# Optimization experiments

Measured on AMD Instinct MI355X. Metric: run time of the kernel, lower is better.

## Reference

```python
import jax, jax.numpy as jnp
import numpy as np

IN_F = 256
OUT_F = 256
HYPER = 128
BATCH = 4096


def setup_inputs() -> dict:
    key = jax.random.key(0)
    ks = jax.random.split(key, 9)
    s_in = 1.0 / np.sqrt(IN_F)
    s_h = 1.0 / np.sqrt(HYPER)
    x = jax.random.normal(ks[0], (BATCH, IN_F), dtype=jnp.float32)
    # weight_gen: Linear(in, hyper) -> ReLU -> Linear(hyper, in*out)
    W1g = jax.random.uniform(ks[1], (IN_F, HYPER), jnp.float32, -s_in, s_in)
    b1g = jax.random.uniform(ks[2], (HYPER,), jnp.float32, -s_in, s_in)
    W2g = jax.random.uniform(ks[3], (HYPER, IN_F * OUT_F), jnp.float32, -s_h, s_h)
    b2g = jax.random.uniform(ks[4], (IN_F * OUT_F,), jnp.float32, -s_h, s_h)
    # bias_gen: Linear(in, hyper) -> ReLU -> Linear(hyper, out)
    W1b = jax.random.uniform(ks[5], (IN_F, HYPER), jnp.float32, -s_in, s_in)
    b1b = jax.random.uniform(ks[6], (HYPER,), jnp.float32, -s_in, s_in)
    W2b = jax.random.uniform(ks[7], (HYPER, OUT_F), jnp.float32, -s_h, s_h)
    b2b = jax.random.uniform(ks[8], (OUT_F,), jnp.float32, -s_h, s_h)
    return {"x": x, "W1g": W1g, "b1g": b1g, "W2g": W2g, "b2g": b2g,
            "W1b": W1b, "b1b": b1b, "W2b": W2b, "b2b": b2b}


def reference(x, W1g, b1g, W2g, b2g, W1b, b1b, W2b, b2b):
    B = x.shape[0]
    # generate per-sample weights [B, out, in]
    hg = jax.nn.relu(x @ W1g + b1g)                      # [B, hyper]
    weights = (hg @ W2g + b2g).reshape(B, OUT_F, IN_F)   # [B, out, in]
    # generate per-sample bias [B, out]
    hb = jax.nn.relu(x @ W1b + b1b)                      # [B, hyper]
    bias = hb @ W2b + b2b                                # [B, out]
    # batched matvec: bmm(weights, x[...,None]) + bias
    out = jnp.einsum('boi,bi->bo', weights, x) + bias    # [B, out]
    return out
```

## Files before the change

kernel.cpp:

```cpp
#include <hip/hip_runtime.h>

#define AS1 __attribute__((address_space(1)))
#define AS3 __attribute__((address_space(3)))

typedef short short8 __attribute__((ext_vector_type(8)));
typedef float f32x16 __attribute__((ext_vector_type(16)));
typedef unsigned short ushort4v __attribute__((ext_vector_type(4)));

#define BATCH 4096
#define IN_F 256
#define OUT_F 256
#define HYP 128
#define HX 129
#define KP (HX * IN_F)

__device__ __forceinline__ float bf2f(unsigned short u) {
  unsigned v = ((unsigned)u) << 16;
  float f;
  __builtin_memcpy(&f, &v, 4);
  return f;
}
__device__ __forceinline__ unsigned short f2bf(float f) {
  unsigned u;
  __builtin_memcpy(&u, &f, 4);
  unsigned r = u + 0x7fffu + ((u >> 16) & 1u);
  return (unsigned short)(r >> 16);
}

__device__ __forceinline__ void gld_lds16(const unsigned short* g, unsigned short* s) {
  __builtin_amdgcn_global_load_lds((const AS1 unsigned int*)g, (AS3 unsigned int*)s, 16, 0, 0);
}

__global__ void k_buildV(const float* __restrict__ W2g, const float* __restrict__ b2g,
                         unsigned short* __restrict__ Vb) {
  const int cid = blockIdx.x * 256 + threadIdx.x;
  const int ic = cid & 31;
  const int pair = cid >> 5;
  const int h = pair % HX;
  const int o = pair / HX;
  const float* src = (h < HYP) ? (W2g + (size_t)h * (OUT_F * IN_F) + o * IN_F + ic * 8)
                               : (b2g + o * IN_F + ic * 8);
  const float4 v0 = ((const float4*)src)[0];
  const float4 v1 = ((const float4*)src)[1];
  uint4 pk;
  pk.x = (unsigned)f2bf(v0.x) | ((unsigned)f2bf(v0.y) << 16);
  pk.y = (unsigned)f2bf(v0.z) | ((unsigned)f2bf(v0.w) << 16);
  pk.z = (unsigned)f2bf(v1.x) | ((unsigned)f2bf(v1.y) << 16);
  pk.w = (unsigned)f2bf(v1.z) | ((unsigned)f2bf(v1.w) << 16);
  *(uint4*)(Vb + (size_t)o * KP + h * IN_F + ic * 8) = pk;
}

__global__ __launch_bounds__(256) void k_pre(const float* __restrict__ x,
                                             const float* __restrict__ W1g, const float* __restrict__ b1g,
                                             const float* __restrict__ W1b, const float* __restrict__ b1b,
                                             const float* __restrict__ W2b, const float* __restrict__ b2b,
                                             unsigned short* __restrict__ hgbT,
                                             unsigned short* __restrict__ xb,
                                             float* __restrict__ out) {
  __shared__ float xl[16 * IN_F];
  __shared__ float hbl[16 * HYP];
  __shared__ unsigned short hgt[HYP * 16];
  const int t = threadIdx.x;
  const int r0 = blockIdx.x * 16;
  for (int j0 = 0; j0 < 16 * IN_F; j0 += 256) {
    const float v = x[(size_t)r0 * IN_F + j0 + t];
    xl[j0 + t] = v;
    xb[(size_t)r0 * IN_F + j0 + t] = f2bf(v);
  }
  __syncthreads();
  const int h = t & 127;
  const int rb = (t >> 7) * 8;
  float ag[8] = {0.f, 0.f, 0.f, 0.f, 0.f, 0.f, 0.f, 0.f};
  float av[8] = {0.f, 0.f, 0.f, 0.f, 0.f, 0.f, 0.f, 0.f};
  for (int i = 0; i < IN_F; ++i) {
    const float wg = W1g[i * HYP + h];
    const float wb = W1b[i * HYP + h];
#pragma unroll
    for (int r = 0; r < 8; ++r) {
      const float xv = xl[(rb + r) * IN_F + i];
      ag[r] += xv * wg;
      av[r] += xv * wb;
    }
  }
  const float bg = b1g[h], bb = b1b[h];
#pragma unroll
  for (int r = 0; r < 8; ++r) {
    float g = ag[r] + bg; g = g > 0.f ? g : 0.f;
    float v = av[r] + bb; v = v > 0.f ? v : 0.f;
    hgt[h * 16 + rb + r] = f2bf(g);
    hbl[(rb + r) * HYP + h] = v;
  }
  __syncthreads();
  {
    const int h2 = t >> 1, part = t & 1;
    const uint4 pk = *(const uint4*)&hgt[h2 * 16 + part * 8];
    *(uint4*)&hgbT[(size_t)h2 * BATCH + r0 + part * 8] = pk;
  }
  float acc[16];
#pragma unroll
  for (int r = 0; r < 16; ++r) acc[r] = 0.f;
  for (int hh = 0; hh < HYP; ++hh) {
    const float w = W2b[hh * OUT_F + t];
#pragma unroll
    for (int r = 0; r < 16; ++r) acc[r] += hbl[r * HYP + hh] * w;
  }
  const float bo = b2b[t];
#pragma unroll
  for (int r = 0; r < 16; ++r) out[(size_t)(r0 + r) * OUT_F + t] = acc[r] + bo;
}

__global__ __launch_bounds__(256, 1) void k_gemm(const unsigned short* __restrict__ Vb,
                                                 const unsigned short* __restrict__ hgbT,
                                                 const unsigned short* __restrict__ xb,
                                                 float* __restrict__ out) {
  __shared__ __align__(16) unsigned short Bl[2][64 * 256];
  __shared__ __align__(16) unsigned short hgs[33 * 256];
  const int tid = threadIdx.x;
  const int lane = tid & 63;
  const int wave = tid >> 6;
  const int l31 = lane & 31;
  const int hi = lane >> 5;
  const int m0 = blockIdx.x * 256;
  const int o0 = blockIdx.y * 64;
  const int z = blockIdx.z;
  const int hBeg = (z * HX) >> 2;
  const int hEnd = ((z + 1) * HX) >> 2;
  const int nh = hEnd - hBeg;

  for (int idx = tid; idx < nh * 256; idx += 256) {
    const int hl = idx >> 8;
    const int hh = hBeg + hl;
    hgs[idx] = (hh == HYP) ? (unsigned short)0x3F80
                           : hgbT[(size_t)hh * BATCH + m0 + (idx & 255)];
  }

  const int mrow0 = m0 + wave * 64 + l31;
  const int mrow1 = mrow0 + 32;
  uint4 xf0[16], xf1[16];
#pragma unroll
  for (int j = 0; j < 16; ++j) {
    xf0[j] = *(const uint4*)(xb + (size_t)mrow0 * IN_F + j * 16 + hi * 8);
    xf1[j] = *(const uint4*)(xb + (size_t)mrow1 * IN_F + j * 16 + hi * 8);
  }

  const int nB = tid >> 5;
  const int p = tid & 31;
  const int cs = p ^ (nB & 7);
  const unsigned short* gsrc = Vb + (size_t)(o0 + nB) * KP + cs * 8 + (size_t)hBeg * IN_F;

  f32x16 zv;
#pragma unroll
  for (int i = 0; i < 16; ++i) zv[i] = 0.0f;
  f32x16 acc00 = zv, acc01 = zv, acc10 = zv, acc11 = zv;
  f32x16 ah00 = zv, ah01 = zv, ah10 = zv, ah11 = zv;

#pragma unroll
  for (int j = 0; j < 8; ++j)
    gld_lds16(gsrc + (size_t)j * 8 * KP, &Bl[0][(tid + 256 * j) * 8]);
  __syncthreads();

  for (int r = 0; r < nh; ++r) {
    const int buf = r & 1;
    if (r + 1 < nh) {
      const unsigned short* gs = gsrc + (size_t)(r + 1) * IN_F;
#pragma unroll
      for (int j = 0; j < 8; ++j)
        gld_lds16(gs + (size_t)j * 8 * KP, &Bl[buf ^ 1][(tid + 256 * j) * 8]);
    }
    float hgf0[16], hgf1[16];
#pragma unroll
    for (int q = 0; q < 4; ++q) {
      const ushort4v v0 = *(const ushort4v*)&hgs[r * 256 + wave * 64 + 4 * hi + q * 8];
      const ushort4v v1 = *(const ushort4v*)&hgs[r * 256 + wave * 64 + 32 + 4 * hi + q * 8];
#pragma unroll
      for (int e = 0; e < 4; ++e) {
        hgf0[q * 4 + e] = bf2f(v0[e]);
        hgf1[q * 4 + e] = bf2f(v1[e]);
      }
    }
    const unsigned short* bp = &Bl[buf][0];
#pragma unroll
    for (int ic = 0; ic < 4; ++ic) {
#pragma unroll
      for (int t = 0; t < 4; ++t) {
        const int c0 = ic * 8 + t * 2 + hi;
        const int pr = c0 ^ (l31 & 7);
        const short8 b0 = *(const short8*)(bp + l31 * 256 + pr * 8);
        const short8 b1 = *(const short8*)(bp + (32 + l31) * 256 + pr * 8);
        const short8 a0 = __builtin_bit_cast(short8, xf0[ic * 4 + t]);
        const short8 a1 = __builtin_bit_cast(short8, xf1[ic * 4 + t]);
        ah00 = __builtin_amdgcn_mfma_f32_32x32x16_bf16(a0, b0, ah00, 0, 0, 0);
        ah01 = __builtin_amdgcn_mfma_f32_32x32x16_bf16(a0, b1, ah01, 0, 0, 0);
        ah10 = __builtin_amdgcn_mfma_f32_32x32x16_bf16(a1, b0, ah10, 0, 0, 0);
        ah11 = __builtin_amdgcn_mfma_f32_32x32x16_bf16(a1, b1, ah11, 0, 0, 0);
      }
    }
#pragma unroll
    for (int g = 0; g < 16; ++g) {
      acc00[g] += hgf0[g] * ah00[g];
      acc01[g] += hgf0[g] * ah01[g];
      acc10[g] += hgf1[g] * ah10[g];
      acc11[g] += hgf1[g] * ah11[g];
    }
    ah00 = zv; ah01 = zv; ah10 = zv; ah11 = zv;
    __syncthreads();
  }

  const int mb = m0 + wave * 64 + 4 * hi;
#pragma unroll
  for (int g = 0; g < 16; ++g) {
    const int row0 = mb + (g & 3) + 8 * (g >> 2);
    atomicAdd(&out[(size_t)row0 * OUT_F + o0 + l31], acc00[g]);
    atomicAdd(&out[(size_t)row0 * OUT_F + o0 + 32 + l31], acc01[g]);
    atomicAdd(&out[(size_t)(row0 + 32) * OUT_F + o0 + l31], acc10[g]);
    atomicAdd(&out[(size_t)(row0 + 32) * OUT_F + o0 + 32 + l31], acc11[g]);
  }
}

extern "C" void kernel_launch(void* const* d_in, const int* in_sizes, int n_in,
                              void* d_out, int out_size, void* d_ws, size_t ws_size,
                              hipStream_t stream) {
  const float* x = (const float*)d_in[0];
  const float* W1g = (const float*)d_in[1];
  const float* b1g = (const float*)d_in[2];
  const float* W2g = (const float*)d_in[3];
  const float* b2g = (const float*)d_in[4];
  const float* W1b = (const float*)d_in[5];
  const float* b1b = (const float*)d_in[6];
  const float* W2b = (const float*)d_in[7];
  const float* b2b = (const float*)d_in[8];
  float* out = (float*)d_out;

  char* ws = (char*)d_ws;
  const size_t szV = (size_t)OUT_F * KP * 2;
  const size_t szHg = (size_t)HYP * BATCH * 2;
  unsigned short* Vb = (unsigned short*)ws;
  unsigned short* hgbT = (unsigned short*)(ws + szV);
  unsigned short* xb = (unsigned short*)(ws + szV + szHg);

  hipLaunchKernelGGL(k_buildV, dim3(OUT_F * HX / 8), dim3(256), 0, stream, W2g, b2g, Vb);
  hipLaunchKernelGGL(k_pre, dim3(BATCH / 16), dim3(256), 0, stream,
                     x, W1g, b1g, W1b, b1b, W2b, b2b, hgbT, xb, out);
  hipLaunchKernelGGL(k_gemm, dim3(BATCH / 256, OUT_F / 64, 4), dim3(256), 0, stream,
                     Vb, hgbT, xb, out);
}
```

Before: 228.1 us.

## Rescale accumulators by hg ratios to chain MFMAs and retile gemm

The gemm no longer forms a per-h partial product and then scales and adds it into the accumulator. It keeps a single running accumulator, multiplies it by hg_prev/hg_next before each new h slice, and applies the final hg once at the end. This lets the MFMAs chain directly into the accumulator and drops the separate partial-sum registers. The hg values are clamped to 1e-20 so the reciprocal stays finite, which adds rounding and underflow risk. The tiling also changes: blocks now cover 32 outputs by 512 batch rows, the K dimension (IN_F) is split in two so the grid becomes 8-deep, occupancy rises to 2 blocks, and the atomic epilogue is transposed through LDS to make the atomics coalesced.

```diff
diff --git a/kernel.cpp b/kernel.cpp
--- a/kernel.cpp
+++ b/kernel.cpp
@@ -5,7 +5,6 @@
 
 typedef short short8 __attribute__((ext_vector_type(8)));
 typedef float f32x16 __attribute__((ext_vector_type(16)));
-typedef unsigned short ushort4v __attribute__((ext_vector_type(4)));
 
 #define BATCH 4096
 #define IN_F 256
@@ -54,7 +53,7 @@
                                              const float* __restrict__ W1g, const float* __restrict__ b1g,
                                              const float* __restrict__ W1b, const float* __restrict__ b1b,
                                              const float* __restrict__ W2b, const float* __restrict__ b2b,
-                                             unsigned short* __restrict__ hgbT,
+                                             unsigned short* __restrict__ hgsT,
                                              unsigned short* __restrict__ xb,
                                              float* __restrict__ out) {
   __shared__ float xl[16 * IN_F];
@@ -87,6 +86,7 @@
   for (int r = 0; r < 8; ++r) {
     float g = ag[r] + bg; g = g > 0.f ? g : 0.f;
     float v = av[r] + bb; v = v > 0.f ? v : 0.f;
+    g = g > 1e-20f ? g : 1e-20f;
     hgt[h * 16 + rb + r] = f2bf(g);
     hbl[(rb + r) * HYP + h] = v;
   }
@@ -94,8 +94,9 @@
   {
     const int h2 = t >> 1, part = t & 1;
     const uint4 pk = *(const uint4*)&hgt[h2 * 16 + part * 8];
-    *(uint4*)&hgbT[(size_t)h2 * BATCH + r0 + part * 8] = pk;
-  }
+    *(uint4*)&hgsT[(size_t)h2 * BATCH + r0 + part * 8] = pk;
+  }
+  if (t < 16) hgsT[(size_t)HYP * BATCH + r0 + t] = 0x3F80;
   float acc[16];
 #pragma unroll
   for (int r = 0; r < 16; ++r) acc[r] = 0.f;
@@ -109,111 +110,122 @@
   for (int r = 0; r < 16; ++r) out[(size_t)(r0 + r) * OUT_F + t] = acc[r] + bo;
 }
 
-__global__ __launch_bounds__(256, 1) void k_gemm(const unsigned short* __restrict__ Vb,
-                                                 const unsigned short* __restrict__ hgbT,
+__global__ __launch_bounds__(256, 2) void k_gemm(const unsigned short* __restrict__ Vb,
+                                                 const unsigned short* __restrict__ hgsT,
                                                  const unsigned short* __restrict__ xb,
                                                  float* __restrict__ out) {
-  __shared__ __align__(16) unsigned short Bl[2][64 * 256];
-  __shared__ __align__(16) unsigned short hgs[33 * 256];
+  __shared__ __align__(16) float smem[512 * 34 + 16];
+  unsigned short* Bl = (unsigned short*)smem;
   const int tid = threadIdx.x;
   const int lane = tid & 63;
   const int wave = tid >> 6;
   const int l31 = lane & 31;
   const int hi = lane >> 5;
-  const int m0 = blockIdx.x * 256;
-  const int o0 = blockIdx.y * 64;
+  const int o0 = blockIdx.x * 32;
+  const int b0 = blockIdx.y * 512;
   const int z = blockIdx.z;
-  const int hBeg = (z * HX) >> 2;
-  const int hEnd = ((z + 1) * HX) >> 2;
+  const int zq = z & 3;
+  const int hBeg = (HX * zq) >> 2;
+  const int hEnd = (HX * (zq + 1)) >> 2;
   const int nh = hEnd - hBeg;
-
-  for (int idx = tid; idx < nh * 256; idx += 256) {
-    const int hl = idx >> 8;
-    const int hh = hBeg + hl;
-    hgs[idx] = (hh == HYP) ? (unsigned short)0x3F80
-                           : hgbT[(size_t)hh * BATCH + m0 + (idx & 255)];
-  }
-
-  const int mrow0 = m0 + wave * 64 + l31;
-  const int mrow1 = mrow0 + 32;
-  uint4 xf0[16], xf1[16];
-#pragma unroll
-  for (int j = 0; j < 16; ++j) {
-    xf0[j] = *(const uint4*)(xb + (size_t)mrow0 * IN_F + j * 16 + hi * 8);
-    xf1[j] = *(const uint4*)(xb + (size_t)mrow1 * IN_F + j * 16 + hi * 8);
-  }
-
-  const int nB = tid >> 5;
-  const int p = tid & 31;
-  const int cs = p ^ (nB & 7);
-  const unsigned short* gsrc = Vb + (size_t)(o0 + nB) * KP + cs * 8 + (size_t)hBeg * IN_F;
+  const int ih = (z >> 2) * 128;
+
+  const int bw = b0 + wave * 128;
+  uint4 xf[4][8];
+#pragma unroll
+  for (int n = 0; n < 4; ++n) {
+    const int brow = bw + n * 32 + l31;
+#pragma unroll
+    for (int t = 0; t < 8; ++t)
+      xf[n][t] = *(const uint4*)(xb + (size_t)brow * IN_F + ih + t * 16 + hi * 8);
+  }
+
+  const int c0 = tid, c1 = tid + 256;
+  const int so0 = c0 >> 4, sp0 = (c0 & 15) ^ (so0 & 15);
+  const int so1 = c1 >> 4, sp1 = (c1 & 15) ^ (so1 & 15);
+  const unsigned short* g0 = Vb + (size_t)(o0 + so0) * KP + ih + sp0 * 8;
+  const unsigned short* g1 = Vb + (size_t)(o0 + so1) * KP + ih + sp1 * 8;
 
   f32x16 zv;
 #pragma unroll
   for (int i = 0; i < 16; ++i) zv[i] = 0.0f;
-  f32x16 acc00 = zv, acc01 = zv, acc10 = zv, acc11 = zv;
-  f32x16 ah00 = zv, ah01 = zv, ah10 = zv, ah11 = zv;
-
-#pragma unroll
-  for (int j = 0; j < 8; ++j)
-    gld_lds16(gsrc + (size_t)j * 8 * KP, &Bl[0][(tid + 256 * j) * 8]);
+  f32x16 acc0 = zv, acc1 = zv, acc2 = zv, acc3 = zv;
+
+  float hgc0 = bf2f(hgsT[(size_t)hBeg * BATCH + bw + 0 * 32 + l31]);
+  float hgc1 = bf2f(hgsT[(size_t)hBeg * BATCH + bw + 1 * 32 + l31]);
+  float hgc2 = bf2f(hgsT[(size_t)hBeg * BATCH + bw + 2 * 32 + l31]);
+  float hgc3 = bf2f(hgsT[(size_t)hBeg * BATCH + bw + 3 * 32 + l31]);
+
+  gld_lds16(g0 + (size_t)hBeg * IN_F, Bl + c0 * 8);
+  gld_lds16(g1 + (size_t)hBeg * IN_F, Bl + c1 * 8);
   __syncthreads();
 
   for (int r = 0; r < nh; ++r) {
+    const int h = hBeg + r;
     const int buf = r & 1;
     if (r + 1 < nh) {
-      const unsigned short* gs = gsrc + (size_t)(r + 1) * IN_F;
-#pragma unroll
-      for (int j = 0; j < 8; ++j)
-        gld_lds16(gs + (size_t)j * 8 * KP, &Bl[buf ^ 1][(tid + 256 * j) * 8]);
-    }
-    float hgf0[16], hgf1[16];
-#pragma unroll
-    for (int q = 0; q < 4; ++q) {
-      const ushort4v v0 = *(const ushort4v*)&hgs[r * 256 + wave * 64 + 4 * hi + q * 8];
-      const ushort4v v1 = *(const ushort4v*)&hgs[r * 256 + wave * 64 + 32 + 4 * hi + q * 8];
-#pragma unroll
-      for (int e = 0; e < 4; ++e) {
-        hgf0[q * 4 + e] = bf2f(v0[e]);
-        hgf1[q * 4 + e] = bf2f(v1[e]);
+      const size_t ko = (size_t)(h + 1) * IN_F;
+      gld_lds16(g0 + ko, Bl + (buf ^ 1) * 4096 + c0 * 8);
+      gld_lds16(g1 + ko, Bl + (buf ^ 1) * 4096 + c1 * 8);
+    }
+    if (r) {
+      const float hn0 = bf2f(hgsT[(size_t)h * BATCH + bw + 0 * 32 + l31]);
+      const float hn1 = bf2f(hgsT[(size_t)h * BATCH + bw + 1 * 32 + l31]);
+      const float hn2 = bf2f(hgsT[(size_t)h * BATCH + bw + 2 * 32 + l31]);
+      const float hn3 = bf2f(hgsT[(size_t)h * BATCH + bw + 3 * 32 + l31]);
+      const float rt0 = hgc0 * __builtin_amdgcn_rcpf(hn0);
+      const float rt1 = hgc1 * __builtin_amdgcn_rcpf(hn1);
+      const float rt2 = hgc2 * __builtin_amdgcn_rcpf(hn2);
+      const float rt3 = hgc3 * __builtin_amdgcn_rcpf(hn3);
+      hgc0 = hn0; hgc1 = hn1; hgc2 = hn2; hgc3 = hn3;
+#pragma unroll
+      for (int g = 0; g < 16; ++g) {
+        acc0[g] *= rt0; acc1[g] *= rt1; acc2[g] *= rt2; acc3[g] *= rt3;
       }
     }
-    const unsigned short* bp = &Bl[buf][0];
-#pragma unroll
-    for (int ic = 0; ic < 4; ++ic) {
-#pragma unroll
-      for (int t = 0; t < 4; ++t) {
-        const int c0 = ic * 8 + t * 2 + hi;
-        const int pr = c0 ^ (l31 & 7);
-        const short8 b0 = *(const short8*)(bp + l31 * 256 + pr * 8);
-        const short8 b1 = *(const short8*)(bp + (32 + l31) * 256 + pr * 8);
-        const short8 a0 = __builtin_bit_cast(short8, xf0[ic * 4 + t]);
-        const short8 a1 = __builtin_bit_cast(short8, xf1[ic * 4 + t]);
-        ah00 = __builtin_amdgcn_mfma_f32_32x32x16_bf16(a0, b0, ah00, 0, 0, 0);
-        ah01 = __builtin_amdgcn_mfma_f32_32x32x16_bf16(a0, b1, ah01, 0, 0, 0);
-        ah10 = __builtin_amdgcn_mfma_f32_32x32x16_bf16(a1, b0, ah10, 0, 0, 0);
-        ah11 = __builtin_amdgcn_mfma_f32_32x32x16_bf16(a1, b1, ah11, 0, 0, 0);
-      }
-    }
-#pragma unroll
-    for (int g = 0; g < 16; ++g) {
-      acc00[g] += hgf0[g] * ah00[g];
-      acc01[g] += hgf0[g] * ah01[g];
-      acc10[g] += hgf1[g] * ah10[g];
-      acc11[g] += hgf1[g] * ah11[g];
-    }
-    ah00 = zv; ah01 = zv; ah10 = zv; ah11 = zv;
+    const unsigned short* bp = Bl + buf * 4096;
+    short8 va[8];
+#pragma unroll
+    for (int t = 0; t < 8; ++t) {
+      const int slot = (t * 2 + hi) ^ (l31 & 15);
+      va[t] = *(const short8*)(bp + l31 * 128 + slot * 8);
+    }
+#pragma unroll
+    for (int t = 0; t < 8; ++t) {
+      acc0 = __builtin_amdgcn_mfma_f32_32x32x16_bf16(va[t], __builtin_bit_cast(short8, xf[0][t]), acc0, 0, 0, 0);
+      acc1 = __builtin_amdgcn_mfma_f32_32x32x16_bf16(va[t], __builtin_bit_cast(short8, xf[1][t]), acc1, 0, 0, 0);
+      acc2 = __builtin_amdgcn_mfma_f32_32x32x16_bf16(va[t], __builtin_bit_cast(short8, xf[2][t]), acc2, 0, 0, 0);
+      acc3 = __builtin_amdgcn_mfma_f32_32x32x16_bf16(va[t], __builtin_bit_cast(short8, xf[3][t]), acc3, 0, 0, 0);
+    }
     __syncthreads();
   }
 
-  const int mb = m0 + wave * 64 + 4 * hi;
 #pragma unroll
   for (int g = 0; g < 16; ++g) {
-    const int row0 = mb + (g & 3) + 8 * (g >> 2);
-    atomicAdd(&out[(size_t)row0 * OUT_F + o0 + l31], acc00[g]);
-    atomicAdd(&out[(size_t)row0 * OUT_F + o0 + 32 + l31], acc01[g]);
-    atomicAdd(&out[(size_t)(row0 + 32) * OUT_F + o0 + l31], acc10[g]);
-    atomicAdd(&out[(size_t)(row0 + 32) * OUT_F + o0 + 32 + l31], acc11[g]);
+    acc0[g] *= hgc0; acc1[g] *= hgc1; acc2[g] *= hgc2; acc3[g] *= hgc3;
+  }
+
+  float* tep = smem;
+#pragma unroll
+  for (int g = 0; g < 16; ++g) {
+    const int orow = (g & 3) + 8 * (g >> 2) + 4 * hi;
+    const int bb = wave * 128;
+    tep[(bb + 0 * 32 + l31) * 34 + orow] = acc0[g];
+    tep[(bb + 1 * 32 + l31) * 34 + orow] = acc1[g];
+    tep[(bb + 2 * 32 + l31) * 34 + orow] = acc2[g];
+    tep[(bb + 3 * 32 + l31) * 34 + orow] = acc3[g];
+  }
+  __syncthreads();
+  const int oq = (tid & 7) * 4;
+  const int br = tid >> 3;
+  for (int it = 0; it < 16; ++it) {
+    const int bl = br + 32 * it;
+    float* op = &out[(size_t)(b0 + bl) * OUT_F + o0 + oq];
+    const float* tp = &tep[bl * 34 + oq];
+    atomicAdd(op + 0, tp[0]);
+    atomicAdd(op + 1, tp[1]);
+    atomicAdd(op + 2, tp[2]);
+    atomicAdd(op + 3, tp[3]);
   }
 }
 
@@ -233,14 +245,14 @@
 
   char* ws = (char*)d_ws;
   const size_t szV = (size_t)OUT_F * KP * 2;
-  const size_t szHg = (size_t)HYP * BATCH * 2;
+  const size_t szHg = (size_t)HX * BATCH * 2;
   unsigned short* Vb = (unsigned short*)ws;
-  unsigned short* hgbT = (unsigned short*)(ws + szV);
+  unsigned short* hgsT = (unsigned short*)(ws + szV);
   unsigned short* xb = (unsigned short*)(ws + szV + szHg);
 
   hipLaunchKernelGGL(k_buildV, dim3(OUT_F * HX / 8), dim3(256), 0, stream, W2g, b2g, Vb);
   hipLaunchKernelGGL(k_pre, dim3(BATCH / 16), dim3(256), 0, stream,
-                     x, W1g, b1g, W1b, b1b, W2b, b2b, hgbT, xb, out);
-  hipLaunchKernelGGL(k_gemm, dim3(BATCH / 256, OUT_F / 64, 4), dim3(256), 0, stream,
-                     Vb, hgbT, xb, out);
-}
+                     x, W1g, b1g, W1b, b1b, W2b, b2b, hgsT, xb, out);
+  hipLaunchKernelGGL(k_gemm, dim3(OUT_F / 32, BATCH / 512, 8), dim3(256), 0, stream,
+                     Vb, hgsT, xb, out);
+}
```

Result: slower. 285.3 us (+25.1%).
